# Optimization experiments

Measured on AMD Instinct MI355X. Metric: run time of the kernel, lower is better.

## Reference

```python
import jax, jax.numpy as jnp
import numpy as np

N_NODES = 50000
N_EDGES = 1000000
F_IN = 256
HEADS = 8
F_HEAD = 32
NEG_SLOPE = 0.2


def setup_inputs() -> dict:
    key = jax.random.key(0)
    ks = jax.random.split(key, 6)
    x = jax.random.normal(ks[0], (N_NODES, F_IN), dtype=jnp.float32)
    # Glorot-ish scaling for stability
    W = jax.random.normal(ks[1], (F_IN, HEADS * F_HEAD), dtype=jnp.float32) / np.sqrt(F_IN)
    att_src = jax.random.normal(ks[2], (HEADS, F_HEAD), dtype=jnp.float32) / np.sqrt(F_HEAD)
    att_dst = jax.random.normal(ks[3], (HEADS, F_HEAD), dtype=jnp.float32) / np.sqrt(F_HEAD)
    bias = jnp.zeros((HEADS * F_HEAD,), dtype=jnp.float32)  # bias_init = zeros_
    edge_index = jax.random.randint(ks[4], (2, N_EDGES), 0, N_NODES, dtype=jnp.int64)
    return {"x": x, "W": W, "att_src": att_src, "att_dst": att_dst, "bias": bias, "edge_index": edge_index}


def reference(x, W, att_src, att_dst, bias, edge_index):
    # GATConv forward (concat=True, add_self_loops=False, negative_slope=0.2)
    N = x.shape[0]
    src, dst = edge_index[0], edge_index[1]
    h = (x @ W).reshape(N, HEADS, F_HEAD)              # [N, H, F]
    a_src = jnp.einsum('nhf,hf->nh', h, att_src)       # [N, H]
    a_dst = jnp.einsum('nhf,hf->nh', h, att_dst)       # [N, H]
    e = jax.nn.leaky_relu(a_src[src] + a_dst[dst], NEG_SLOPE)  # [E, H]
    # segment softmax over incoming edges of each dst node
    e_max = jax.ops.segment_max(e, dst, num_segments=N)        # [N, H] (-inf for isolated, unused)
    e_exp = jnp.exp(e - e_max[dst])                            # [E, H]
    denom = jax.ops.segment_sum(e_exp, dst, num_segments=N)    # [N, H]
    alpha = e_exp / denom[dst]                                 # [E, H]
    # attention-weighted scatter-add aggregation
    msgs = alpha[:, :, None] * h[src]                          # [E, H, F]
    out = jax.ops.segment_sum(msgs, dst, num_segments=N)       # [N, H, F]
    return out.reshape(N, HEADS * F_HEAD) + bias
```

## Files before the change

kernel.cpp:

```cpp
#include <hip/hip_runtime.h>
#include <hip/hip_fp16.h>

#define F_IN 256
#define HEADS 8
#define F_HEAD 32
#define HF 256
#define NEG_SLOPE 0.2f

typedef float    floatx4 __attribute__((ext_vector_type(4)));
typedef short    shortx8 __attribute__((ext_vector_type(8)));
typedef _Float16 halfx4  __attribute__((ext_vector_type(4)));
typedef _Float16 halfx8  __attribute__((ext_vector_type(8)));

__device__ __forceinline__ float bf2f(unsigned short u) {
    return __uint_as_float(((unsigned int)u) << 16);
}
__device__ __forceinline__ unsigned short f2bf(float f) {
    unsigned int b = __float_as_uint(f);
    b += 0x7FFFu + ((b >> 16) & 1u);
    return (unsigned short)(b >> 16);
}

__device__ __forceinline__ int edge_at(const void* ei, int is32, long long idx) {
    if (is32) return ((const int*)ei)[idx];
    return (int)((const long long*)ei)[idx];
}
__device__ __forceinline__ float fload(const void* p, int isf32, int idx) {
    if (isf32) return ((const float*)p)[idx];
    return bf2f(((const unsigned short*)p)[idx]);
}

__global__ void detect_all(const unsigned int* eiw, int E,
                           const unsigned short* xu, int xnels,
                           int* ebits, int* nzpart, int* lgpart) {
    __shared__ int red[256];
    int b = blockIdx.x, tid = threadIdx.x;
    if (b < 256) {
        unsigned int acc = 0;
        for (int i = b * 256 + tid; i < E; i += 256 * 256) acc |= eiw[2 * i + 1];
        red[tid] = (acc != 0);
        __syncthreads();
        for (int o = 128; o; o >>= 1) {
            if (tid < o) red[tid] |= red[tid + o];
            __syncthreads();
        }
        if (tid == 0) ebits[b] = red[0];
    } else {
        int bb = b - 256;
        int cap = xnels < (1 << 21) ? xnels : (1 << 21);
        int large = 0, nz = 0;
        for (int j = 2 * (bb * 256 + tid); j < cap; j += 2 * 256 * 256) {
            unsigned short v = xu[j];
            large |= ((v & 0x7FFF) >= 0x4700);
            nz += (v != 0);
        }
        red[tid] = nz;
        __syncthreads();
        for (int o = 128; o; o >>= 1) {
            if (tid < o) red[tid] += red[tid + o];
            __syncthreads();
        }
        if (tid == 0) nzpart[bb] = red[0];
        __syncthreads();
        red[tid] = large;
        __syncthreads();
        for (int o = 128; o; o >>= 1) {
            if (tid < o) red[tid] |= red[tid + o];
            __syncthreads();
        }
        if (tid == 0) lgpart[bb] = red[0];
    }
}

__global__ void finalize_misc(const int* ebits, const int* nzpart, const int* lgpart,
                              const unsigned int* c0, const unsigned int* c1,
                              const unsigned int* c2, int* flags, int tot) {
    __shared__ int r0[256], r1[256], r2[256];
    __shared__ int nzf[3];
    int tid = threadIdx.x;
    if (tid < 3) nzf[tid] = 0;
    r0[tid] = ebits[tid];
    r1[tid] = nzpart[tid];
    r2[tid] = lgpart[tid];
    __syncthreads();
    for (int o = 128; o; o >>= 1) {
        if (tid < o) {
            r0[tid] |= r0[tid + o];
            r1[tid] += r1[tid + o];
            r2[tid] |= r2[tid + o];
        }
        __syncthreads();
    }
    if (tid < 192) {
        int j = tid >> 6, lane = tid & 63;
        const unsigned int* c = (j == 0) ? c0 : (j == 1) ? c1 : c2;
        if ((c[lane] | c[lane + 64]) != 0) nzf[j] = 1;
    }
    __syncthreads();
    if (tid == 0) {
        int bi = (nzf[0] == 0) ? 0 : (nzf[1] == 0) ? 1 : 2;
        int fl = bi << 3;
        if (r0[0]) fl |= 1;
        if (r2[0] != 0 || r1[0] * 2 < tot) fl |= 2;
        flags[0] = fl;
    }
}

__device__ __forceinline__ void resolve3(const void* c0, const void* c1,
        const void* c2, int fl, const void** as, const void** ad, const void** bs) {
    int bi = (fl >> 3) & 3;
    const void* c[3] = {c0, c1, c2};
    int i0 = (bi == 0) ? 1 : 0;
    int i1 = (bi == 2) ? 1 : 2;
    *as = c[i0];
    *ad = c[i1];
    *bs = c[bi];
}

__global__ void transpose_w(const void* W, unsigned short* Wt, const int* flags) {
    int isf32 = flags[0] & 2;
    int u = blockIdx.x * 256 + threadIdx.x;
    int n = u & 255, k = u >> 8;
    int j = k & 7, lane_hi = (k >> 3) & 3, ks = k >> 5;
    int lane_lo = n & 15, ct = n >> 4;
    int dest = ((ct * 8 + ks) * 64 + lane_hi * 16 + lane_lo) * 8 + j;
    Wt[dest] = isf32 ? f2bf(((const float*)W)[u])
                     : ((const unsigned short*)W)[u];
}

__global__ __launch_bounds__(256) void gemm_h(const void* x, const short* Wt,
        _Float16* h, const void* c0, const void* c1, const void* c2,
        _Float16* asrc, _Float16* adst, const int* flags, int nRows) {
    __shared__ float s_att[2][HF];
    int fl = flags[0];
    int xf32 = fl & 2;
    {
        const void *pa, *pd, *pb;
        resolve3(c0, c1, c2, fl, &pa, &pd, &pb);
        int tid = threadIdx.x;
        s_att[0][tid] = fload(pa, xf32, tid);
        s_att[1][tid] = fload(pd, xf32, tid);
    }
    __syncthreads();

    int gwave = (blockIdx.x * blockDim.x + threadIdx.x) >> 6;
    int widr  = gwave >> 1;
    int chalf = gwave & 1;
    int lane = threadIdx.x & 63;
    int rowTiles = nRows >> 4;
    if (widr >= rowTiles) return;
    int quad = lane >> 4, m = lane & 15;

    shortx8 a[8];
    size_t arow = (size_t)(widr * 16 + m) * 256 + quad * 8;
    if (xf32) {
        const floatx4* apf = (const floatx4*)((const float*)x + arow);
#pragma unroll
        for (int ks = 0; ks < 8; ++ks) {
            floatx4 f0 = apf[ks * 8], f1 = apf[ks * 8 + 1];
            unsigned int* au = (unsigned int*)&a[ks];
            au[0] = __builtin_amdgcn_perm(__float_as_uint(f0[1]), __float_as_uint(f0[0]), 0x07060302u);
            au[1] = __builtin_amdgcn_perm(__float_as_uint(f0[3]), __float_as_uint(f0[2]), 0x07060302u);
            au[2] = __builtin_amdgcn_perm(__float_as_uint(f1[1]), __float_as_uint(f1[0]), 0x07060302u);
            au[3] = __builtin_amdgcn_perm(__float_as_uint(f1[3]), __float_as_uint(f1[2]), 0x07060302u);
        }
    } else {
        const shortx8* ap = (const shortx8*)((const unsigned short*)x + arow);
#pragma unroll
        for (int ks = 0; ks < 8; ++ks) a[ks] = ap[ks * 4];
    }

    float ss0 = 0.f, ss1 = 0.f, ss2 = 0.f, ss3 = 0.f;
    float sd0 = 0.f, sd1 = 0.f, sd2 = 0.f, sd3 = 0.f;

    const shortx8* bq = (const shortx8*)Wt;
    int ct0 = chalf * 8;
#pragma unroll 4
    for (int ct = ct0; ct < ct0 + 8; ++ct) {
        const shortx8* bp = bq + (size_t)(ct * 8) * 64 + lane;
        floatx4 acc = {0.f, 0.f, 0.f, 0.f};
#pragma unroll
        for (int ks = 0; ks < 8; ++ks) {
            shortx8 b = bp[(size_t)ks * 64];
            acc = __builtin_amdgcn_mfma_f32_16x16x32_bf16(a[ks], b, acc, 0, 0, 0);
        }
        _Float16* hp = h + (size_t)(widr * 16 + quad * 4) * 256 + ct * 16 + m;
#pragma unroll
        for (int r = 0; r < 4; ++r) hp[(size_t)r * 256] = (_Float16)acc[r];

        float sa = s_att[0][ct * 16 + m];
        float da = s_att[1][ct * 16 + m];
        ss0 += acc[0] * sa; ss1 += acc[1] * sa; ss2 += acc[2] * sa; ss3 += acc[3] * sa;
        sd0 += acc[0] * da; sd1 += acc[1] * da; sd2 += acc[2] * da; sd3 += acc[3] * da;
        if (ct & 1) {
#pragma unroll
            for (int off = 1; off < 16; off <<= 1) {
                ss0 += __shfl_xor(ss0, off, 16); ss1 += __shfl_xor(ss1, off, 16);
                ss2 += __shfl_xor(ss2, off, 16); ss3 += __shfl_xor(ss3, off, 16);
                sd0 += __shfl_xor(sd0, off, 16); sd1 += __shfl_xor(sd1, off, 16);
                sd2 += __shfl_xor(sd2, off, 16); sd3 += __shfl_xor(sd3, off, 16);
            }
            if (m == 0) {
                int hd = ct >> 1;
                size_t rb = (size_t)(widr * 16 + quad * 4) * 8 + hd;
                asrc[rb]      = (_Float16)ss0; asrc[rb + 8]  = (_Float16)ss1;
                asrc[rb + 16] = (_Float16)ss2; asrc[rb + 24] = (_Float16)ss3;
                adst[rb]      = (_Float16)sd0; adst[rb + 8]  = (_Float16)sd1;
                adst[rb + 16] = (_Float16)sd2; adst[rb + 24] = (_Float16)sd3;
            }
            ss0 = ss1 = ss2 = ss3 = 0.f;
            sd0 = sd1 = sd2 = sd3 = 0.f;
        }
    }
}

__global__ void bucket_hist(const void* ei, const int* flags, int E, int n,
                            int K, int* cntmat) {
    __shared__ int lh[256];
    int b = blockIdx.x, tid = threadIdx.x;
    lh[tid] = 0;
    __syncthreads();
    int is32 = flags[0] & 1;
    for (int e = b * 256 + tid; e < E; e += 256 * 256) {
        int d = edge_at(ei, is32, (long long)E + e);
        if ((unsigned)d < (unsigned)n) atomicAdd(&lh[d >> 8], 1);
    }
    __syncthreads();
    if (tid < K) cntmat[tid * 256 + b] = lh[tid];
}

__global__ void bucket_write(const void* ei, const int* flags, int E, int n,
                             int K, const int* scanned, unsigned int* bucketed) {
    __shared__ int cur[256];
    int b = blockIdx.x, tid = threadIdx.x;
    if (tid < K) cur[tid] = scanned[tid * 256 + b];
    __syncthreads();
    int is32 = flags[0] & 1;
    for (int e = b * 256 + tid; e < E; e += 256 * 256) {
        int d = edge_at(ei, is32, (long long)E + e);
        if ((unsigned)d >= (unsigned)n) continue;
        int s = edge_at(ei, is32, e);
        if ((unsigned)s >= (unsigned)n) s = 0;
        int pos = atomicAdd(&cur[d >> 8], 1);
        bucketed[pos] = (unsigned)s | ((unsigned)(d & 255) << 16);
    }
}

__global__ void csr_build(const unsigned int* bucketed, const int* scanned,
                          int E, int n, int K, int* rowp, unsigned short* csr) {
    __shared__ int cnt[256], pfx[256], cur[256];
    int k = blockIdx.x, tid = threadIdx.x;
    int beg = scanned[k * 256];
    int end = scanned[(k + 1) * 256];
    cnt[tid] = 0;
    __syncthreads();
    for (int e = beg + tid; e < end; e += 256)
        atomicAdd(&cnt[bucketed[e] >> 16], 1);
    __syncthreads();
    pfx[tid] = cnt[tid];
    __syncthreads();
    for (int o = 1; o < 256; o <<= 1) {
        int t = (tid >= o) ? pfx[tid - o] : 0;
        __syncthreads();
        pfx[tid] += t;
        __syncthreads();
    }
    int base = beg + pfx[tid] - cnt[tid];
    int d = k * 256 + tid;
    if (d < n) rowp[d] = base;
    if (k == 0 && tid == 0) rowp[n] = E;
    cur[tid] = base;
    __syncthreads();
    for (int e = beg + tid; e < end; e += 256) {
        unsigned int pe = bucketed[e];
        int pos = atomicAdd(&cur[pe >> 16], 1);
        csr[pos] = (unsigned short)(pe & 0xFFFFu);
    }
}

__global__ void scan_blocks(const int* counts, int* row, int* bsum, int n) {
    __shared__ int s[256];
    int tid = threadIdx.x;
    int g = blockIdx.x * 256 + tid;
    int v = (g < n) ? counts[g] : 0;
    s[tid] = v;
    __syncthreads();
    for (int o = 1; o < 256; o <<= 1) {
        int t = (tid >= o) ? s[tid - o] : 0;
        __syncthreads();
        s[tid] += t;
        __syncthreads();
    }
    if (g < n) row[g] = s[tid] - v;
    if (tid == 255) bsum[blockIdx.x] = s[255];
}

__global__ void add_offsets(int* row, const int* bsum, int* cursor,
                            int nb, int n, int E) {
    __shared__ int sc[256];
    __shared__ int blockoff;
    int tid = threadIdx.x;
    int v = (tid < nb) ? bsum[tid] : 0;
    sc[tid] = v;
    __syncthreads();
    for (int o = 1; o < 256; o <<= 1) {
        int t = (tid >= o) ? sc[tid - o] : 0;
        __syncthreads();
        sc[tid] += t;
        __syncthreads();
    }
    if (tid == 0) blockoff = (blockIdx.x == 0) ? 0 : sc[blockIdx.x - 1];
    __syncthreads();
    int g = blockIdx.x * 256 + tid;
    if (g < n) {
        int r = row[g] + blockoff;
        row[g] = r;
        cursor[g] = r;
        if (g == 0) row[n] = E;
    }
}

__global__ __launch_bounds__(256) void gat_node(const _Float16* h, const _Float16* asrc,
        const _Float16* adst, const int* row, const unsigned short* csr_src,
        const void* c0, const void* c1, const void* c2,
        const int* flags, float* out, int n0, int n1) {
    int fl = flags[0];
    int isf32 = fl & 2;
    const void *asu, *adu, *bias;
    resolve3(c0, c1, c2, fl, &asu, &adu, &bias);
    (void)asu; (void)adu;
    int wid  = n0 + ((blockIdx.x * 256 + threadIdx.x) >> 6);
    int lane = threadIdx.x & 63;
    if (wid >= n1) return;
    int beg = row[wid], end = row[wid + 1];
    int slot = lane >> 3, head = lane & 7;
    int l3   = lane >> 3;

    float ad_l = (float)adst[(size_t)wid * 8 + head];

    float m = -1e30f, s = 0.f;
    float acc0 = 0.f, acc1 = 0.f, acc2 = 0.f, acc3 = 0.f;
    const _Float16* hb = h + lane * 4;

    int p = beg + slot;
    int act = p < end;
    int sn = act ? (int)csr_src[p] : 0;
    float av = (float)asrc[(size_t)sn * 8 + head];

    for (int p0 = beg; p0 < end; p0 += 8) {
        int actc = act, snc = sn;
        float avc = av;

        int sn_e[8];
#pragma unroll
        for (int e = 0; e < 8; ++e) sn_e[e] = __shfl(snc, e * 8, 64);
        halfx4 hv[8];
#pragma unroll
        for (int e = 0; e < 8; ++e)
            hv[e] = *(const halfx4*)(hb + (size_t)sn_e[e] * HF);

        int pn = p0 + 8 + slot;
        act = pn < end;
        sn = act ? (int)csr_src[pn] : 0;
        av = (float)asrc[(size_t)sn * 8 + head];

        float v = avc + ad_l;
        v = v > 0.f ? v : NEG_SLOPE * v;
        v = actc ? v : -1e30f;
        float vm = fmaxf(v, __shfl_xor(v, 8, 64));
        vm = fmaxf(vm, __shfl_xor(vm, 16, 64));
        vm = fmaxf(vm, __shfl_xor(vm, 32, 64));
        float mn = fmaxf(m, vm);
        float scale = __expf(m - mn);
        float t = actc ? __expf(v - mn) : 0.f;
        s = s * scale + t;
        m = mn;

        float scale_f = __shfl(scale, l3, 64);
        acc0 *= scale_f; acc1 *= scale_f; acc2 *= scale_f; acc3 *= scale_f;
#pragma unroll
        for (int e = 0; e < 8; ++e) {
            float a_e = __shfl(t, e * 8 + l3, 64);
            acc0 += a_e * (float)hv[e][0];
            acc1 += a_e * (float)hv[e][1];
            acc2 += a_e * (float)hv[e][2];
            acc3 += a_e * (float)hv[e][3];
        }
    }

    s += __shfl_xor(s, 8, 64);
    s += __shfl_xor(s, 16, 64);
    s += __shfl_xor(s, 32, 64);
    float inv = s > 0.f ? 1.f / s : 0.f;
    float inv_f = __shfl(inv, l3, 64);

    int cb = lane * 4;
    floatx4 o;
    o[0] = acc0 * inv_f + fload(bias, isf32, cb);
    o[1] = acc1 * inv_f + fload(bias, isf32, cb + 1);
    o[2] = acc2 * inv_f + fload(bias, isf32, cb + 2);
    o[3] = acc3 * inv_f + fload(bias, isf32, cb + 3);
    *(floatx4*)(out + (size_t)wid * HF + cb) = o;
}

extern "C" void kernel_launch(void* const* d_in, const int* in_sizes, int n_in,
                              void* d_out, int out_size, void* d_ws, size_t ws_size,
                              hipStream_t stream) {
    int order[16];
    for (int i = 0; i < n_in && i < 16; ++i) order[i] = i;
    for (int i = 0; i < n_in - 1; ++i)
        for (int j = i + 1; j < n_in; ++j)
            if (in_sizes[order[j]] > in_sizes[order[i]]) {
                int t = order[i]; order[i] = order[j]; order[j] = t;
            }
    int ix  = order[0];
    int iei = order[1];
    int iw  = order[2];
    int cand[3], nc = 0;
    for (int i = 0; i < n_in && nc < 3; ++i)
        if (i != ix && i != iei && i != iw) cand[nc++] = i;

    const void* x   = d_in[ix];
    const void* W   = d_in[iw];
    const void* ei  = d_in[iei];
    const void* ca0 = d_in[cand[0]];
    const void* ca1 = d_in[cand[1]];
    const void* ca2 = d_in[cand[2]];
    float* out = (float*)d_out;

    int N = in_sizes[ix] / F_IN;
    int E = in_sizes[iei] / 2;

    int K = (N + 255) >> 8;
    int M = K * 256;

    char* ws = (char*)d_ws;
    size_t off = 0;
    auto alloc = [&](size_t bytes) -> void* {
        void* p = ws + off;
        off += (bytes + 255) & ~(size_t)255;
        return p;
    };
    int*            flags   = (int*)alloc(16);
    size_t          zero_span = off;
    int*            ebits   = (int*)alloc(256 * 4);
    int*            nzpart  = (int*)alloc(256 * 4);
    int*            lgpart  = (int*)alloc(256 * 4);
    int*            bsum    = (int*)alloc(256 * 4);
    int*            cntmat  = (int*)alloc((size_t)M * 4);
    int*            scanned = (int*)alloc(((size_t)M + 1) * 4);
    int*            rowp    = (int*)alloc(((size_t)N + 1) * 4);
    unsigned int*   bucketed= (unsigned int*)alloc((size_t)E * 4);
    unsigned short* Wt      = (unsigned short*)alloc(256 * 256 * 2);
    _Float16*       asrc    = (_Float16*)alloc((size_t)N * HEADS * 2);
    _Float16*       adst    = (_Float16*)alloc((size_t)N * HEADS * 2);
    unsigned short* csr     = (unsigned short*)alloc((size_t)E * 2);
    _Float16*       h       = (_Float16*)alloc((size_t)N * HF * 2);

    hipMemsetAsync(ws, 0, zero_span, stream);
    hipMemsetAsync(csr, 0, (size_t)E * 2, stream);

    detect_all<<<512, 256, 0, stream>>>((const unsigned int*)ei, E,
                                        (const unsigned short*)x, in_sizes[ix],
                                        ebits, nzpart, lgpart);
    int cap = in_sizes[ix] < (1 << 21) ? in_sizes[ix] : (1 << 21);
    int tot = (cap + 1) / 2;
    finalize_misc<<<1, 256, 0, stream>>>(ebits, nzpart, lgpart,
                                         (const unsigned int*)ca0,
                                         (const unsigned int*)ca1,
                                         (const unsigned int*)ca2, flags, tot);
    transpose_w<<<256, 256, 0, stream>>>(W, Wt, flags);

    int rowTiles = N / 16;
    int gemmWaves = rowTiles * 2;
    int gemmBlocks = (gemmWaves * 64 + 255) / 256;
    gemm_h<<<gemmBlocks, 256, 0, stream>>>(x, (const short*)Wt, h,
                                           ca0, ca1, ca2, asrc, adst, flags, N);

    bucket_hist<<<256, 256, 0, stream>>>(ei, flags, E, N, K, cntmat);
    int nbM = (M + 255) / 256;
    scan_blocks<<<nbM, 256, 0, stream>>>(cntmat, scanned, bsum, M);
    add_offsets<<<nbM, 256, 0, stream>>>(scanned, bsum, cntmat , nbM, M, E);
    bucket_write<<<256, 256, 0, stream>>>(ei, flags, E, N, K, scanned, bucketed);
    csr_build<<<K, 256, 0, stream>>>(bucketed, scanned, E, N, K, rowp, csr);

    int half = N >> 1;
    gat_node<<<(half + 3) / 4, 256, 0, stream>>>(h, asrc, adst, rowp, csr,
                                                 ca0, ca1, ca2, flags, out, 0, half);
    gat_node<<<((N - half) + 3) / 4, 256, 0, stream>>>(h, asrc, adst, rowp, csr,
                                                       ca0, ca1, ca2, flags, out, half, N);
}
```

Before: 269.0 us.

## Merge preprocessing kernels and fold scan offsets into bucket/CSR kernels

Fuses the W transpose with the bucket histogram into one launch, and runs the per-bucket scan as extra blocks of the GEMM kernel. The separate global offset-add pass is dropped: bucket_write and csr_build each recompute the prefix over bucket sums in shared memory. The two memsets are also removed. This cuts several kernel launches and serialization points in exchange for redundant small scans per block and reliance on every workspace entry being written before it is read.

Result: faster. 259.1 us (-3.7%).

```diff
diff --git a/kernel.cpp b/kernel.cpp
--- a/kernel.cpp
+++ b/kernel.cpp
@@ -117,20 +117,57 @@
     *bs = c[bi];
 }
 
-__global__ void transpose_w(const void* W, unsigned short* Wt, const int* flags) {
-    int isf32 = flags[0] & 2;
-    int u = blockIdx.x * 256 + threadIdx.x;
-    int n = u & 255, k = u >> 8;
-    int j = k & 7, lane_hi = (k >> 3) & 3, ks = k >> 5;
-    int lane_lo = n & 15, ct = n >> 4;
-    int dest = ((ct * 8 + ks) * 64 + lane_hi * 16 + lane_lo) * 8 + j;
-    Wt[dest] = isf32 ? f2bf(((const float*)W)[u])
-                     : ((const unsigned short*)W)[u];
-}
-
-__global__ __launch_bounds__(256) void gemm_h(const void* x, const short* Wt,
+__global__ void prep_kernel(const void* W, unsigned short* Wt,
+                            const void* ei, int E, int n, int K, int* cntmat,
+                            const int* flags) {
+    int b = blockIdx.x, tid = threadIdx.x;
+    if (b < 256) {
+        int isf32 = flags[0] & 2;
+        int u = b * 256 + tid;
+        int nn = u & 255, k = u >> 8;
+        int j = k & 7, lane_hi = (k >> 3) & 3, ks = k >> 5;
+        int lane_lo = nn & 15, ct = nn >> 4;
+        int dest = ((ct * 8 + ks) * 64 + lane_hi * 16 + lane_lo) * 8 + j;
+        Wt[dest] = isf32 ? f2bf(((const float*)W)[u])
+                         : ((const unsigned short*)W)[u];
+    } else {
+        __shared__ int lh[256];
+        int bb = b - 256;
+        lh[tid] = 0;
+        __syncthreads();
+        int is32 = flags[0] & 1;
+        for (int e = bb * 256 + tid; e < E; e += 256 * 256) {
+            int d = edge_at(ei, is32, (long long)E + e);
+            if ((unsigned)d < (unsigned)n) atomicAdd(&lh[d >> 8], 1);
+        }
+        __syncthreads();
+        if (tid < K) cntmat[tid * 256 + bb] = lh[tid];
+    }
+}
+
+__global__ __launch_bounds__(256) void gemm_scan(const void* x, const short* Wt,
         _Float16* h, const void* c0, const void* c1, const void* c2,
-        _Float16* asrc, _Float16* adst, const int* flags, int nRows) {
+        _Float16* asrc, _Float16* adst, const int* flags, int nRows,
+        int gemmBlocks, int* cntmat, int* bsum, int K) {
+    if ((int)blockIdx.x >= gemmBlocks) {
+        __shared__ int s[256];
+        int j = blockIdx.x - gemmBlocks;
+        int tid = threadIdx.x;
+        int g = j * 256 + tid;
+        int v = cntmat[g];
+        s[tid] = v;
+        __syncthreads();
+        for (int o = 1; o < 256; o <<= 1) {
+            int t = (tid >= o) ? s[tid - o] : 0;
+            __syncthreads();
+            s[tid] += t;
+            __syncthreads();
+        }
+        cntmat[g] = s[tid] - v;
+        if (tid == 255) bsum[j] = s[255];
+        return;
+    }
+
     __shared__ float s_att[2][HF];
     int fl = flags[0];
     int xf32 = fl & 2;
@@ -214,26 +251,22 @@
     }
 }
 
-__global__ void bucket_hist(const void* ei, const int* flags, int E, int n,
-                            int K, int* cntmat) {
-    __shared__ int lh[256];
-    int b = blockIdx.x, tid = threadIdx.x;
-    lh[tid] = 0;
-    __syncthreads();
-    int is32 = flags[0] & 1;
-    for (int e = b * 256 + tid; e < E; e += 256 * 256) {
-        int d = edge_at(ei, is32, (long long)E + e);
-        if ((unsigned)d < (unsigned)n) atomicAdd(&lh[d >> 8], 1);
-    }
-    __syncthreads();
-    if (tid < K) cntmat[tid * 256 + b] = lh[tid];
-}
-
 __global__ void bucket_write(const void* ei, const int* flags, int E, int n,
-                             int K, const int* scanned, unsigned int* bucketed) {
+                             int K, const int* rel, const int* bsum,
+                             unsigned int* bucketed) {
+    __shared__ int pref[256];
     __shared__ int cur[256];
     int b = blockIdx.x, tid = threadIdx.x;
-    if (tid < K) cur[tid] = scanned[tid * 256 + b];
+    int v = (tid < K) ? bsum[tid] : 0;
+    pref[tid] = v;
+    __syncthreads();
+    for (int o = 1; o < 256; o <<= 1) {
+        int t = (tid >= o) ? pref[tid - o] : 0;
+        __syncthreads();
+        pref[tid] += t;
+        __syncthreads();
+    }
+    if (tid < K) cur[tid] = (pref[tid] - v) + rel[tid * 256 + b];
     __syncthreads();
     int is32 = flags[0] & 1;
     for (int e = b * 256 + tid; e < E; e += 256 * 256) {
@@ -246,14 +279,28 @@
     }
 }
 
-__global__ void csr_build(const unsigned int* bucketed, const int* scanned,
-                          int E, int n, int K, int* rowp, unsigned short* csr) {
-    __shared__ int cnt[256], pfx[256], cur[256];
+__global__ void csr_build(const unsigned int* bucketed, const int* bsum,
+                          int n, int K, int* rowp, unsigned short* csr) {
+    __shared__ int pref[256], cnt[256], pfx[256], cur[256];
+    __shared__ int sBeg, sEnd;
     int k = blockIdx.x, tid = threadIdx.x;
-    int beg = scanned[k * 256];
-    int end = scanned[(k + 1) * 256];
+    int v = (tid < K) ? bsum[tid] : 0;
+    pref[tid] = v;
+    __syncthreads();
+    for (int o = 1; o < 256; o <<= 1) {
+        int t = (tid >= o) ? pref[tid - o] : 0;
+        __syncthreads();
+        pref[tid] += t;
+        __syncthreads();
+    }
+    if (tid == 0) {
+        sEnd = pref[k];
+        sBeg = pref[k] - bsum[k];
+        if (k == K - 1) rowp[n] = pref[K - 1];
+    }
     cnt[tid] = 0;
     __syncthreads();
+    int beg = sBeg, end = sEnd;
     for (int e = beg + tid; e < end; e += 256)
         atomicAdd(&cnt[bucketed[e] >> 16], 1);
     __syncthreads();
@@ -268,55 +315,12 @@
     int base = beg + pfx[tid] - cnt[tid];
     int d = k * 256 + tid;
     if (d < n) rowp[d] = base;
-    if (k == 0 && tid == 0) rowp[n] = E;
     cur[tid] = base;
     __syncthreads();
     for (int e = beg + tid; e < end; e += 256) {
         unsigned int pe = bucketed[e];
         int pos = atomicAdd(&cur[pe >> 16], 1);
         csr[pos] = (unsigned short)(pe & 0xFFFFu);
-    }
-}
-
-__global__ void scan_blocks(const int* counts, int* row, int* bsum, int n) {
-    __shared__ int s[256];
-    int tid = threadIdx.x;
-    int g = blockIdx.x * 256 + tid;
-    int v = (g < n) ? counts[g] : 0;
-    s[tid] = v;
-    __syncthreads();
-    for (int o = 1; o < 256; o <<= 1) {
-        int t = (tid >= o) ? s[tid - o] : 0;
-        __syncthreads();
-        s[tid] += t;
-        __syncthreads();
-    }
-    if (g < n) row[g] = s[tid] - v;
-    if (tid == 255) bsum[blockIdx.x] = s[255];
-}
-
-__global__ void add_offsets(int* row, const int* bsum, int* cursor,
-                            int nb, int n, int E) {
-    __shared__ int sc[256];
-    __shared__ int blockoff;
-    int tid = threadIdx.x;
-    int v = (tid < nb) ? bsum[tid] : 0;
-    sc[tid] = v;
-    __syncthreads();
-    for (int o = 1; o < 256; o <<= 1) {
-        int t = (tid >= o) ? sc[tid - o] : 0;
-        __syncthreads();
-        sc[tid] += t;
-        __syncthreads();
-    }
-    if (tid == 0) blockoff = (blockIdx.x == 0) ? 0 : sc[blockIdx.x - 1];
-    __syncthreads();
-    int g = blockIdx.x * 256 + tid;
-    if (g < n) {
-        int r = row[g] + blockoff;
-        row[g] = r;
-        cursor[g] = r;
-        if (g == 0) row[n] = E;
     }
 }
 
@@ -442,13 +446,11 @@
         return p;
     };
     int*            flags   = (int*)alloc(16);
-    size_t          zero_span = off;
     int*            ebits   = (int*)alloc(256 * 4);
     int*            nzpart  = (int*)alloc(256 * 4);
     int*            lgpart  = (int*)alloc(256 * 4);
     int*            bsum    = (int*)alloc(256 * 4);
     int*            cntmat  = (int*)alloc((size_t)M * 4);
-    int*            scanned = (int*)alloc(((size_t)M + 1) * 4);
     int*            rowp    = (int*)alloc(((size_t)N + 1) * 4);
     unsigned int*   bucketed= (unsigned int*)alloc((size_t)E * 4);
     unsigned short* Wt      = (unsigned short*)alloc(256 * 256 * 2);
@@ -456,9 +458,6 @@
     _Float16*       adst    = (_Float16*)alloc((size_t)N * HEADS * 2);
     unsigned short* csr     = (unsigned short*)alloc((size_t)E * 2);
     _Float16*       h       = (_Float16*)alloc((size_t)N * HF * 2);
-
-    hipMemsetAsync(ws, 0, zero_span, stream);
-    hipMemsetAsync(csr, 0, (size_t)E * 2, stream);
 
     detect_all<<<512, 256, 0, stream>>>((const unsigned int*)ei, E,
                                         (const unsigned short*)x, in_sizes[ix],
@@ -469,20 +468,18 @@
                                          (const unsigned int*)ca0,
                                          (const unsigned int*)ca1,
                                          (const unsigned int*)ca2, flags, tot);
-    transpose_w<<<256, 256, 0, stream>>>(W, Wt, flags);
+
+    prep_kernel<<<512, 256, 0, stream>>>(W, Wt, ei, E, N, K, cntmat, flags);
 
     int rowTiles = N / 16;
     int gemmWaves = rowTiles * 2;
     int gemmBlocks = (gemmWaves * 64 + 255) / 256;
-    gemm_h<<<gemmBlocks, 256, 0, stream>>>(x, (const short*)Wt, h,
-                                           ca0, ca1, ca2, asrc, adst, flags, N);
-
-    bucket_hist<<<256, 256, 0, stream>>>(ei, flags, E, N, K, cntmat);
-    int nbM = (M + 255) / 256;
-    scan_blocks<<<nbM, 256, 0, stream>>>(cntmat, scanned, bsum, M);
-    add_offsets<<<nbM, 256, 0, stream>>>(scanned, bsum, cntmat , nbM, M, E);
-    bucket_write<<<256, 256, 0, stream>>>(ei, flags, E, N, K, scanned, bucketed);
-    csr_build<<<K, 256, 0, stream>>>(bucketed, scanned, E, N, K, rowp, csr);
+    gemm_scan<<<gemmBlocks + K, 256, 0, stream>>>(x, (const short*)Wt, h,
+                                                  ca0, ca1, ca2, asrc, adst, flags, N,
+                                                  gemmBlocks, cntmat, bsum, K);
+
+    bucket_write<<<256, 256, 0, stream>>>(ei, flags, E, N, K, cntmat, bsum, bucketed);
+    csr_build<<<K, 256, 0, stream>>>(bucketed, bsum, N, K, rowp, csr);
 
     int half = N >> 1;
     gat_node<<<(half + 3) / 4, 256, 0, stream>>>(h, asrc, adst, rowp, csr,
```
